# Kernel tuning notes

Hardware: AMD Instinct MI355X
Metric: run time of the kernel (lower is better)

## Reference

```python
import jax, jax.numpy as jnp
import numpy as np

N_NODES = 50000
N_EDGES = 800000
IN_F, H_F, OUT_F = 256, 256, 128


def setup_inputs() -> dict:
    key = jax.random.key(0)
    k1, k2, k3, k4, k5, k6 = jax.random.split(key, 6)
    in_feat = jax.random.normal(k1, (N_NODES, IN_F), dtype=jnp.float32)
    src = jax.random.randint(k2, (N_EDGES,), 0, N_NODES, dtype=jnp.int32)
    dst = jax.random.randint(k3, (N_EDGES,), 0, N_NODES, dtype=jnp.int32)
    s1 = 1.0 / np.sqrt(IN_F)
    s2 = 1.0 / np.sqrt(H_F)
    W1 = jax.random.uniform(k4, (IN_F, H_F), dtype=jnp.float32, minval=-s1, maxval=s1)
    b1 = jnp.zeros((H_F,), dtype=jnp.float32)
    W2 = jax.random.uniform(k5, (H_F, OUT_F), dtype=jnp.float32, minval=-s2, maxval=s2)
    b2 = jnp.zeros((OUT_F,), dtype=jnp.float32)
    return {"in_feat": in_feat, "src": src, "dst": dst,
            "W1": W1, "b1": b1, "W2": W2, "b2": b2}


def _graph_conv(x, W, b, src, dst, n_nodes):
    # DGL GraphConv with norm='both':
    #   h = D_in^{-1/2} A D_out^{-1/2} (X W) + b   (degrees clamped to min 1)
    ones = jnp.ones((src.shape[0],), dtype=x.dtype)
    deg_out = jax.ops.segment_sum(ones, src, num_segments=n_nodes)
    deg_in = jax.ops.segment_sum(ones, dst, num_segments=n_nodes)
    norm_out = jax.lax.rsqrt(jnp.maximum(deg_out, 1.0))  # [N]
    norm_in = jax.lax.rsqrt(jnp.maximum(deg_in, 1.0))    # [N]
    h = (x @ W) * norm_out[:, None]                       # [N, F_out]
    agg = jax.ops.segment_sum(h[src], dst, num_segments=n_nodes)  # SpMM
    return agg * norm_in[:, None] + b


def reference(in_feat, src, dst, W1, b1, W2, b2):
    n = in_feat.shape[0]
    h = _graph_conv(in_feat, W1, b1, src, dst, n)
    h = jax.nn.relu(h)
    h = _graph_conv(h, W2, b2, src, dst, n)
    # dgl.mean_nodes over a single graph -> mean across all nodes
    return jnp.mean(h, axis=0)  # [OUT_F]
```

## Files before the change

### kernel.cpp

```cpp
#include <hip/hip_runtime.h>


#define NNODES 50000
#define NEDGES 800000
#define CH      64
#define EPC     (NEDGES / CH)
#define NVEC    12
#define TAILB   (NVEC * 1024)
#define TAILN   (EPC - TAILB)
#define HWORDS  12500
#define QN      12500
#define G1_BM   ((NNODES + 127) / 128)
#define MEGA_NB 768
#define WS_NB   1536
#define NQUAD   (NNODES / 4)

typedef __bf16 bf16x8 __attribute__((ext_vector_type(8)));
typedef float f32x4 __attribute__((ext_vector_type(4)));
typedef float f32x2 __attribute__((ext_vector_type(2)));

__device__ __forceinline__ unsigned short f2b(float f) {
    union { float f; unsigned u; } v; v.f = f;
    unsigned r = 0x7fffu + ((v.u >> 16) & 1u);
    return (unsigned short)((v.u + r) >> 16);
}
__device__ __forceinline__ unsigned char f2fp8(float x) {
    return (unsigned char)(__builtin_amdgcn_cvt_pk_fp8_f32(x, x, 0, false) & 0xff);
}
__device__ __forceinline__ float rdeg(int d) {
    return __frsqrt_rn((float)max(d, 1));
}

__global__ __launch_bounds__(256) void k_hist0(
    const float* __restrict__ W1, unsigned short* __restrict__ W1t,
    const int* __restrict__ src, const int* __restrict__ dst,
    unsigned* __restrict__ degInP,
    unsigned* __restrict__ degOutP)
{
    __shared__ unsigned lds[HWORDS];
    int bid = blockIdx.x, tid = threadIdx.x;

    if (bid < 256) {
        int id = bid * 256 + tid;
        int k = id >> 8, n = id & 255;
        W1t[n * 256 + k] = f2b(W1[id]);
        return;
    }

    int b = bid - 256;
    const int* key = (b < 128) ? dst : src;
    unsigned* outP = (b < 128) ? degInP : degOutP;
    int b2 = b & 127;
    int c = b2 >> 1, h = b2 & 1;
    int lo = h * 25000;

    for (int i = tid; i < HWORDS; i += 256) lds[i] = 0;
    __syncthreads();
    int base = c * EPC;
    for (int i = 0; i < NVEC; i++) {
        int e = base + (i * 256 + tid) * 4;
        int4 k4 = *(const int4*)&key[e];
        int kk[4] = {k4.x, k4.y, k4.z, k4.w};
#pragma unroll
        for (int u = 0; u < 4; u++) {
            unsigned r = (unsigned)(kk[u] - lo);
            if (r < 25000u) atomicAdd(&lds[r >> 1], 1u << ((r & 1) * 16));
        }
    }
    if (tid < TAILN) {
        unsigned r = (unsigned)(key[base + TAILB + tid] - lo);
        if (r < 25000u) atomicAdd(&lds[r >> 1], 1u << ((r & 1) * 16));
    }
    __syncthreads();
    unsigned* op = outP + (size_t)b2 * HWORDS;
    for (int i = tid; i < HWORDS; i += 256) op[i] = lds[i];
}

__global__ __launch_bounds__(256) void k_merge0(
    const unsigned* __restrict__ degInP, const unsigned* __restrict__ degOutP,
    unsigned* __restrict__ chunkStartPk,
    float* __restrict__ normIn, float* __restrict__ normOut,
    int* __restrict__ degc)
{
    int id = blockIdx.x * blockDim.x + threadIdx.x;
    if (id >= 25000) return;
    int h = id >= HWORDS, w = id - h * HWORDS;
    unsigned runLo = 0, runHi = 0, oLo = 0, oHi = 0;
#pragma unroll 8
    for (int c = 0; c < CH; c++) {
        size_t idx = (size_t)(c * 2 + h) * HWORDS + w;
        unsigned x = degInP[idx];
        chunkStartPk[idx] = runLo | (runHi << 16);
        runLo += x & 0xffffu; runHi += x >> 16;
        unsigned y = degOutP[idx];
        oLo += y & 0xffffu; oHi += y >> 16;
    }
    int d0 = h * 25000 + 2 * w, d1 = d0 + 1;
    normIn[d0] = rdeg((int)runLo);  normIn[d1] = rdeg((int)runHi);
    normOut[d0] = rdeg((int)oLo);   normOut[d1] = rdeg((int)oHi);
    degc[d0] = min((int)runLo, 64); degc[d1] = min((int)runHi, 64);
}

__global__ __launch_bounds__(256) void k_mega2(
    const int* __restrict__ src, const int* __restrict__ dst,
    const unsigned* __restrict__ chunkStartPk,
    unsigned short* __restrict__ col2,
    const float* __restrict__ normIn, const float* __restrict__ normOut,
    float* __restrict__ wsumP,
    const float* __restrict__ X, const unsigned short* __restrict__ W1t,
    unsigned char* __restrict__ H, int M)
{
    __shared__ __align__(16) unsigned char smem[50048];
    int bid = blockIdx.x, tid = threadIdx.x;

    if (bid < 128) {
        unsigned* cntL = (unsigned*)smem;
        int c = bid >> 1, h = bid & 1;
        int lo = h * 25000;
        const unsigned* cs = chunkStartPk + (size_t)(c * 2 + h) * HWORDS;
        for (int i = tid; i < HWORDS; i += 256) cntL[i] = cs[i];
        __syncthreads();
        int base = c * EPC;
        for (int i = 0; i < NVEC; i++) {
            int e = base + (i * 256 + tid) * 4;
            int4 d4 = *(const int4*)&dst[e];
            int4 s4 = *(const int4*)&src[e];
            int dd[4] = {d4.x, d4.y, d4.z, d4.w};
            int ss[4] = {s4.x, s4.y, s4.z, s4.w};
#pragma unroll
            for (int u = 0; u < 4; u++) {
                unsigned r = (unsigned)(dd[u] - lo);
                if (r < 25000u) {
                    unsigned sh = (r & 1) * 16;
                    unsigned wv = atomicAdd(&cntL[r >> 1], 1u << sh);
                    unsigned slot = (wv >> sh) & 0xffffu;
                    if (slot < 64) col2[(size_t)dd[u] * 64 + slot] = (unsigned short)ss[u];
                }
            }
        }
        if (tid < TAILN) {
            int e = base + TAILB + tid;
            int d = dst[e];
            unsigned r = (unsigned)(d - lo);
            if (r < 25000u) {
                int s = src[e];
                unsigned sh = (r & 1) * 16;
                unsigned wv = atomicAdd(&cntL[r >> 1], 1u << sh);
                unsigned slot = (wv >> sh) & 0xffffu;
                if (slot < 64) col2[(size_t)d * 64 + slot] = (unsigned short)s;
            }
        }
        return;
    }

    if (bid < 384) {
        float* wf = (float*)smem;
        int b2 = bid - 128;
        int c = b2 >> 2, q = b2 & 3;
        int lo = q * QN;
        for (int i = tid; i < QN; i += 256) wf[i] = 0.f;
        __syncthreads();
        int base = c * EPC;
        for (int i = 0; i < NVEC; i++) {
            int e = base + (i * 256 + tid) * 4;
            int4 s4 = *(const int4*)&src[e];
            int4 d4 = *(const int4*)&dst[e];
            int ss[4] = {s4.x, s4.y, s4.z, s4.w};
            int dd[4] = {d4.x, d4.y, d4.z, d4.w};
#pragma unroll
            for (int u = 0; u < 4; u++) {
                unsigned r = (unsigned)(ss[u] - lo);
                if (r < (unsigned)QN) {
                    float ni = normIn[dd[u]];
                    atomicAdd(&wf[r], ni);
                }
            }
        }
        if (tid < TAILN) {
            int e = base + TAILB + tid;
            unsigned r = (unsigned)(src[e] - lo);
            if (r < (unsigned)QN) atomicAdd(&wf[r], normIn[dst[e]]);
        }
        __syncthreads();
        float* op = wsumP + (size_t)b2 * QN;
        for (int i = tid; i < QN; i += 256) op[i] = wf[i];
        return;
    }

    unsigned short (*As)[40] = (unsigned short (*)[40])smem;
    unsigned short (*Bs)[40] = (unsigned short (*)[40])(smem + 10240);
    int lane = tid & 63, wave = tid >> 6;
    int wm = (wave >> 1) * 64, wn = (wave & 1) * 64;
    int q = lane >> 4, r16 = lane & 15;
    int c0 = tid, c1 = tid + 256;
    int r0 = c0 >> 2, k0c = (c0 & 3) * 8;
    int r1 = c1 >> 2, k1c = (c1 & 3) * 8;

    auto pk2u = [](float a, float b) -> unsigned {
        unsigned short x = f2b(a), y = f2b(b);
        return (unsigned)x | ((unsigned)y << 16);
    };

    for (int g = bid - 384; g < 2 * G1_BM; g += MEGA_NB - 384) {
        int bm = g % G1_BM, bn = g / G1_BM;
        int m0 = bm * 128, n0 = bn * 128;

        f32x4 acc[4][4];
#pragma unroll
        for (int i = 0; i < 4; i++)
#pragma unroll
            for (int j = 0; j < 4; j++) acc[i][j] = 0.f;

        const float* Ar0 = X + (size_t)min(m0 + r0, M - 1) * 256;
        const float* Ar1 = X + (size_t)min(m0 + r1, M - 1) * 256;
        const unsigned short* Br0 = W1t + (size_t)(n0 + r0) * 256;
        const unsigned short* Br1 = W1t + (size_t)(n0 + r1) * 256;

        for (int k0 = 0; k0 < 256; k0 += 32) {
            float4 fa0 = *(const float4*)(Ar0 + k0 + k0c);
            float4 fa1 = *(const float4*)(Ar0 + k0 + k0c + 4);
            float4 fb0 = *(const float4*)(Ar1 + k0 + k1c);
            float4 fb1 = *(const float4*)(Ar1 + k0 + k1c + 4);
            uint4 vb0 = *(const uint4*)(Br0 + k0 + k0c);
            uint4 vb1 = *(const uint4*)(Br1 + k0 + k1c);
            uint4 va0 = make_uint4(pk2u(fa0.x, fa0.y), pk2u(fa0.z, fa0.w), pk2u(fa1.x, fa1.y), pk2u(fa1.z, fa1.w));
            uint4 va1 = make_uint4(pk2u(fb0.x, fb0.y), pk2u(fb0.z, fb0.w), pk2u(fb1.x, fb1.y), pk2u(fb1.z, fb1.w));
            __syncthreads();
            *(uint4*)&As[r0][k0c] = va0;
            *(uint4*)&As[r1][k1c] = va1;
            *(uint4*)&Bs[r0][k0c] = vb0;
            *(uint4*)&Bs[r1][k1c] = vb1;
            __syncthreads();
            bf16x8 af[4], bf[4];
#pragma unroll
            for (int i = 0; i < 4; i++)
                af[i] = *(const bf16x8*)&As[wm + i * 16 + r16][q * 8];
#pragma unroll
            for (int j = 0; j < 4; j++)
                bf[j] = *(const bf16x8*)&Bs[wn + j * 16 + r16][q * 8];
#pragma unroll
            for (int i = 0; i < 4; i++)
#pragma unroll
                for (int j = 0; j < 4; j++)
                    acc[i][j] = __builtin_amdgcn_mfma_f32_16x16x32_bf16(af[i], bf[j], acc[i][j], 0, 0, 0);
        }

#pragma unroll
        for (int i = 0; i < 4; i++) {
#pragma unroll
            for (int rr = 0; rr < 4; rr++) {
                int m = m0 + wm + i * 16 + q * 4 + rr;
                if (m < M) {
                    float no = normOut[m];
                    unsigned char* Hp = H + (size_t)m * 256 + n0 + wn + r16;
#pragma unroll
                    for (int j = 0; j < 4; j++)
                        Hp[j * 16] = f2fp8(acc[i][j][rr] * no);
                }
            }
        }
    }
}

__global__ __launch_bounds__(256) void k_merge1(
    const float* __restrict__ wsumP, const float* __restrict__ normOut,
    const float* __restrict__ normIn, const int* __restrict__ degc,
    float4* __restrict__ meta)
{
    int i = blockIdx.x * blockDim.x + threadIdx.x;
    if (i >= NNODES) return;
    int q = i / QN, li = i - q * QN;
    float ws = 0.f;
#pragma unroll 8
    for (int c = 0; c < CH; c++) ws += wsumP[(size_t)(c * 4 + q) * QN + li];
    meta[i] = make_float4(normOut[i] * ws, normIn[i],
                          __int_as_float(degc[i]), 0.f);
}

__global__ __launch_bounds__(256) void k_spmm_wsum(
    const unsigned char* __restrict__ H, const float4* __restrict__ meta,
    const unsigned short* __restrict__ col2,
    const float* __restrict__ bias, float* __restrict__ vpart) {
    __shared__ float sm[4][256];
    int wave = threadIdx.x >> 6;
    int lane = threadIdx.x & 63;
    int f = lane * 4;
    const unsigned char* Hf = H + f;
    float4 bv = *(const float4*)(bias + f);
    float vac0 = 0.f, vac1 = 0.f, vac2 = 0.f, vac3 = 0.f;

    int qd = blockIdx.x;
    int node = qd * 4 + wave;
    float4 pM = make_float4(0.f, 0.f, 0.f, 0.f);
    int pc = 0;
    if (qd < NQUAD) {
        pM = meta[node];
        pc = (int)col2[(size_t)node * 64 + lane];
    }

    while (qd < NQUAD) {
        float wn = pM.x, nI = pM.y;
        int dI = __float_as_int(pM.z), myc = pc;

        int nqd = qd + gridDim.x;
        if (nqd < NQUAD) {
            int nn = nqd * 4 + wave;
            pM = meta[nn];
            pc = (int)col2[(size_t)nn * 64 + lane];
        }

        float a0 = 0.f, a1 = 0.f, a2 = 0.f, a3 = 0.f;
        int i = 0;
        for (; i + 16 <= dI; i += 16) {
            unsigned v[16];
#pragma unroll
            for (int u = 0; u < 16; u++) {
                int c = __builtin_amdgcn_readlane(myc, i + u);
                v[u] = *(const unsigned*)(Hf + (size_t)c * 256);
            }
#pragma unroll
            for (int u = 0; u < 16; u++) {
                f32x2 lo = __builtin_amdgcn_cvt_pk_f32_fp8(v[u], false);
                f32x2 hi = __builtin_amdgcn_cvt_pk_f32_fp8(v[u], true);
                a0 += lo.x; a1 += lo.y; a2 += hi.x; a3 += hi.y;
            }
        }
        for (; i + 4 <= dI; i += 4) {
            unsigned v[4];
#pragma unroll
            for (int u = 0; u < 4; u++) {
                int c = __builtin_amdgcn_readlane(myc, i + u);
                v[u] = *(const unsigned*)(Hf + (size_t)c * 256);
            }
#pragma unroll
            for (int u = 0; u < 4; u++) {
                f32x2 lo = __builtin_amdgcn_cvt_pk_f32_fp8(v[u], false);
                f32x2 hi = __builtin_amdgcn_cvt_pk_f32_fp8(v[u], true);
                a0 += lo.x; a1 += lo.y; a2 += hi.x; a3 += hi.y;
            }
        }
        for (; i < dI; i++) {
            int c = __builtin_amdgcn_readlane(myc, i);
            unsigned v = *(const unsigned*)(Hf + (size_t)c * 256);
            f32x2 lo = __builtin_amdgcn_cvt_pk_f32_fp8(v, false);
            f32x2 hi = __builtin_amdgcn_cvt_pk_f32_fp8(v, true);
            a0 += lo.x; a1 += lo.y; a2 += hi.x; a3 += hi.y;
        }

        vac0 += wn * fmaxf(a0 * nI + bv.x, 0.f);
        vac1 += wn * fmaxf(a1 * nI + bv.y, 0.f);
        vac2 += wn * fmaxf(a2 * nI + bv.z, 0.f);
        vac3 += wn * fmaxf(a3 * nI + bv.w, 0.f);

        qd = nqd;
    }

    *(float4*)&sm[wave][f] = make_float4(vac0, vac1, vac2, vac3);
    __syncthreads();
    int t = threadIdx.x;
    float s4 = sm[0][t] + sm[1][t] + sm[2][t] + sm[3][t];
    vpart[(size_t)blockIdx.x * 256 + t] = s4;
}

__global__ __launch_bounds__(256) void k_red1(const float* __restrict__ vpart,
                                              float* __restrict__ vred) {
    int b = blockIdx.x;
    int t = threadIdx.x;
    float s = 0.f;
    for (int i = b; i < WS_NB; i += 64) s += vpart[(size_t)i * 256 + t];
    vred[(size_t)b * 256 + t] = s;
}

__global__ __launch_bounds__(1024) void k_final(
    const float* __restrict__ vred, const float* __restrict__ W2,
    const float* __restrict__ b2, float* __restrict__ out) {
    __shared__ float part[4][256];
    __shared__ float v[256];
    int t = threadIdx.x;
    int feat = t & 255, pr = t >> 8;
    float s = 0.f;
    for (int i = pr; i < 64; i += 4) s += vred[(size_t)i * 256 + feat];
    part[pr][feat] = s;
    __syncthreads();
    if (t < 256) v[t] = part[0][t] + part[1][t] + part[2][t] + part[3][t];
    __syncthreads();
    if (t < 128) {
        float o = 0.f;
        for (int k = 0; k < 256; k++) o += v[k] * W2[k * 128 + t];
        out[t] = o * (1.0f / (float)NNODES) + b2[t];
    }
}

extern "C" void kernel_launch(void* const* d_in, const int* in_sizes, int n_in,
                              void* d_out, int out_size, void* d_ws, size_t ws_size,
                              hipStream_t stream) {
    const float* X   = (const float*)d_in[0];
    const int*   src = (const int*)d_in[1];
    const int*   dst = (const int*)d_in[2];
    const float* W1  = (const float*)d_in[3];
    const float* b1  = (const float*)d_in[4];
    const float* W2  = (const float*)d_in[5];
    const float* b2  = (const float*)d_in[6];
    float* out = (float*)d_out;

    const int n = NNODES;

    char* p = (char*)d_ws;
    auto carve = [&](size_t bytes) -> void* {
        void* r = (void*)p;
        p += (bytes + 255) & ~(size_t)255;
        return r;
    };
    unsigned short* col2 = (unsigned short*)carve((size_t)n * 64 * 2);
    unsigned short* W1t  = (unsigned short*)carve((size_t)256 * 256 * 2);
    unsigned char*  bufA = (unsigned char*)carve((size_t)n * 256);
    float* normIn  = (float*)carve((size_t)n * sizeof(float));
    float* normOut = (float*)carve((size_t)n * sizeof(float));
    int*   degc    = (int*)carve((size_t)n * sizeof(int));
    float4* meta   = (float4*)carve((size_t)n * sizeof(float4));
    size_t histP_bytes = (size_t)128 * HWORDS * sizeof(unsigned);
    char* histr = (char*)carve(2 * histP_bytes);
    unsigned* degInP  = (unsigned*)histr;
    unsigned* degOutP = (unsigned*)(histr + histP_bytes);
    float*    wsumP   = (float*)histr;
    char* csr = (char*)carve(histP_bytes);
    unsigned* chunkStartPk = (unsigned*)csr;
    float* vpart = (float*)csr;
    float* vred  = (float*)(csr + (size_t)WS_NB * 256 * sizeof(float));

    k_hist0<<<512, 256, 0, stream>>>(W1, W1t, src, dst, degInP, degOutP);

    k_merge0<<<98, 256, 0, stream>>>(degInP, degOutP, chunkStartPk,
                                     normIn, normOut, degc);

    k_mega2<<<MEGA_NB, 256, 0, stream>>>(
        src, dst, chunkStartPk, col2, normIn, normOut, wsumP, X, W1t, bufA, n);

    k_merge1<<<(n + 255) / 256, 256, 0, stream>>>(wsumP, normOut, normIn, degc, meta);

    k_spmm_wsum<<<WS_NB, 256, 0, stream>>>(bufA, meta, col2, b1, vpart);

    k_red1<<<64, 256, 0, stream>>>(vpart, vred);
    k_final<<<1, 1024, 0, stream>>>(vred, W2, b2, out);
}
```

Baseline: 214.3 us.

## Partition SpMM gather into source-range passes and give GEMM one tile per block

The SpMM kernel now gives each block up to 8 node-quads and makes 4 passes over their neighbour lists. Each pass gathers only source rows from one quarter of the node range, so the working set of H per pass is smaller and more likely to stay in cache. The GEMM part of the mega kernel drops its grid-stride loop and launches enough blocks for one output tile each. The cost is redundant readlane and predicate work across passes and more registers for the 8 accumulators, which can lower occupancy. Per-iteration loads are also predicated and no longer batched, which reduces memory-level parallelism.

```diff
diff --git a/kernel.cpp b/kernel.cpp
--- a/kernel.cpp
+++ b/kernel.cpp
@@ -11,9 +11,11 @@
 #define HWORDS  12500
 #define QN      12500
 #define G1_BM   ((NNODES + 127) / 128)
-#define MEGA_NB 768
-#define WS_NB   1536
+#define MEGA_NB (128 + 256 + 2 * G1_BM)
+#define WS_NB   1563
 #define NQUAD   (NNODES / 4)
+#define NPASS   4
+#define PQ      12500
 
 typedef __bf16 bf16x8 __attribute__((ext_vector_type(8)));
 typedef float f32x4 __attribute__((ext_vector_type(4)));
@@ -189,74 +191,72 @@
 
     unsigned short (*As)[40] = (unsigned short (*)[40])smem;
     unsigned short (*Bs)[40] = (unsigned short (*)[40])(smem + 10240);
+    int g = bid - 384;
+    int bm = g % G1_BM, bn = g / G1_BM;
+    int m0 = bm * 128, n0 = bn * 128;
     int lane = tid & 63, wave = tid >> 6;
     int wm = (wave >> 1) * 64, wn = (wave & 1) * 64;
     int q = lane >> 4, r16 = lane & 15;
+
+    f32x4 acc[4][4];
+#pragma unroll
+    for (int i = 0; i < 4; i++)
+#pragma unroll
+        for (int j = 0; j < 4; j++) acc[i][j] = 0.f;
+
     int c0 = tid, c1 = tid + 256;
     int r0 = c0 >> 2, k0c = (c0 & 3) * 8;
     int r1 = c1 >> 2, k1c = (c1 & 3) * 8;
+    const float* Ar0 = X + (size_t)min(m0 + r0, M - 1) * 256;
+    const float* Ar1 = X + (size_t)min(m0 + r1, M - 1) * 256;
+    const unsigned short* Br0 = W1t + (size_t)(n0 + r0) * 256;
+    const unsigned short* Br1 = W1t + (size_t)(n0 + r1) * 256;
 
     auto pk2u = [](float a, float b) -> unsigned {
         unsigned short x = f2b(a), y = f2b(b);
         return (unsigned)x | ((unsigned)y << 16);
     };
 
-    for (int g = bid - 384; g < 2 * G1_BM; g += MEGA_NB - 384) {
-        int bm = g % G1_BM, bn = g / G1_BM;
-        int m0 = bm * 128, n0 = bn * 128;
-
-        f32x4 acc[4][4];
+    for (int k0 = 0; k0 < 256; k0 += 32) {
+        float4 fa0 = *(const float4*)(Ar0 + k0 + k0c);
+        float4 fa1 = *(const float4*)(Ar0 + k0 + k0c + 4);
+        float4 fb0 = *(const float4*)(Ar1 + k0 + k1c);
+        float4 fb1 = *(const float4*)(Ar1 + k0 + k1c + 4);
+        uint4 vb0 = *(const uint4*)(Br0 + k0 + k0c);
+        uint4 vb1 = *(const uint4*)(Br1 + k0 + k1c);
+        uint4 va0 = make_uint4(pk2u(fa0.x, fa0.y), pk2u(fa0.z, fa0.w), pk2u(fa1.x, fa1.y), pk2u(fa1.z, fa1.w));
+        uint4 va1 = make_uint4(pk2u(fb0.x, fb0.y), pk2u(fb0.z, fb0.w), pk2u(fb1.x, fb1.y), pk2u(fb1.z, fb1.w));
+        __syncthreads();
+        *(uint4*)&As[r0][k0c] = va0;
+        *(uint4*)&As[r1][k1c] = va1;
+        *(uint4*)&Bs[r0][k0c] = vb0;
+        *(uint4*)&Bs[r1][k1c] = vb1;
+        __syncthreads();
+        bf16x8 af[4], bf[4];
 #pragma unroll
         for (int i = 0; i < 4; i++)
-#pragma unroll
-            for (int j = 0; j < 4; j++) acc[i][j] = 0.f;
-
-        const float* Ar0 = X + (size_t)min(m0 + r0, M - 1) * 256;
-        const float* Ar1 = X + (size_t)min(m0 + r1, M - 1) * 256;
-        const unsigned short* Br0 = W1t + (size_t)(n0 + r0) * 256;
-        const unsigned short* Br1 = W1t + (size_t)(n0 + r1) * 256;
-
-        for (int k0 = 0; k0 < 256; k0 += 32) {
-            float4 fa0 = *(const float4*)(Ar0 + k0 + k0c);
-            float4 fa1 = *(const float4*)(Ar0 + k0 + k0c + 4);
-            float4 fb0 = *(const float4*)(Ar1 + k0 + k1c);
-            float4 fb1 = *(const float4*)(Ar1 + k0 + k1c + 4);
-            uint4 vb0 = *(const uint4*)(Br0 + k0 + k0c);
-            uint4 vb1 = *(const uint4*)(Br1 + k0 + k1c);
-            uint4 va0 = make_uint4(pk2u(fa0.x, fa0.y), pk2u(fa0.z, fa0.w), pk2u(fa1.x, fa1.y), pk2u(fa1.z, fa1.w));
-            uint4 va1 = make_uint4(pk2u(fb0.x, fb0.y), pk2u(fb0.z, fb0.w), pk2u(fb1.x, fb1.y), pk2u(fb1.z, fb1.w));
-            __syncthreads();
-            *(uint4*)&As[r0][k0c] = va0;
-            *(uint4*)&As[r1][k1c] = va1;
-            *(uint4*)&Bs[r0][k0c] = vb0;
-            *(uint4*)&Bs[r1][k1c] = vb1;
-            __syncthreads();
-            bf16x8 af[4], bf[4];
-#pragma unroll
-            for (int i = 0; i < 4; i++)
-                af[i] = *(const bf16x8*)&As[wm + i * 16 + r16][q * 8];
+            af[i] = *(const bf16x8*)&As[wm + i * 16 + r16][q * 8];
+#pragma unroll
+        for (int j = 0; j < 4; j++)
+            bf[j] = *(const bf16x8*)&Bs[wn + j * 16 + r16][q * 8];
+#pragma unroll
+        for (int i = 0; i < 4; i++)
 #pragma unroll
             for (int j = 0; j < 4; j++)
-                bf[j] = *(const bf16x8*)&Bs[wn + j * 16 + r16][q * 8];
-#pragma unroll
-            for (int i = 0; i < 4; i++)
+                acc[i][j] = __builtin_amdgcn_mfma_f32_16x16x32_bf16(af[i], bf[j], acc[i][j], 0, 0, 0);
+    }
+
+#pragma unroll
+    for (int i = 0; i < 4; i++) {
+#pragma unroll
+        for (int rr = 0; rr < 4; rr++) {
+            int m = m0 + wm + i * 16 + q * 4 + rr;
+            if (m < M) {
+                float no = normOut[m];
+                unsigned char* Hp = H + (size_t)m * 256 + n0 + wn + r16;
 #pragma unroll
                 for (int j = 0; j < 4; j++)
-                    acc[i][j] = __builtin_amdgcn_mfma_f32_16x16x32_bf16(af[i], bf[j], acc[i][j], 0, 0, 0);
-        }
-
-#pragma unroll
-        for (int i = 0; i < 4; i++) {
-#pragma unroll
-            for (int rr = 0; rr < 4; rr++) {
-                int m = m0 + wm + i * 16 + q * 4 + rr;
-                if (m < M) {
-                    float no = normOut[m];
-                    unsigned char* Hp = H + (size_t)m * 256 + n0 + wn + r16;
-#pragma unroll
-                    for (int j = 0; j < 4; j++)
-                        Hp[j * 16] = f2fp8(acc[i][j][rr] * no);
-                }
+                    Hp[j * 16] = f2fp8(acc[i][j][rr] * no);
             }
         }
     }
@@ -279,87 +279,75 @@
 
 __global__ __launch_bounds__(256) void k_spmm_wsum(
     const unsigned char* __restrict__ H, const float4* __restrict__ meta,
-    const unsigned short* __restrict__ col2,
+    const int* __restrict__ degc, const unsigned short* __restrict__ col2,
     const float* __restrict__ bias, float* __restrict__ vpart) {
     __shared__ float sm[4][256];
     int wave = threadIdx.x >> 6;
     int lane = threadIdx.x & 63;
     int f = lane * 4;
     const unsigned char* Hf = H + f;
+    int bid = blockIdx.x;
+
+    int colr[8];
+    int di[8];
+    float a[8][4];
+#pragma unroll
+    for (int qi = 0; qi < 8; qi++) {
+        int qd = bid + qi * WS_NB;
+        colr[qi] = 0; di[qi] = 0;
+        a[qi][0] = a[qi][1] = a[qi][2] = a[qi][3] = 0.f;
+        if (qd < NQUAD) {
+            int node = qd * 4 + wave;
+            di[qi] = degc[node];
+            colr[qi] = (int)col2[(size_t)node * 64 + lane];
+        }
+    }
+
+    for (int p = 0; p < NPASS; p++) {
+        int plo = p * PQ;
+#pragma unroll
+        for (int qi = 0; qi < 8; qi++) {
+            int dI = di[qi];
+            int myc = colr[qi];
+            for (int i = 0; i < dI; i += 16) {
+#pragma unroll
+                for (int u = 0; u < 16; u++) {
+                    if (i + u < dI) {
+                        int c = __builtin_amdgcn_readlane(myc, i + u);
+                        if ((unsigned)(c - plo) < (unsigned)PQ) {
+                            unsigned v = *(const unsigned*)(Hf + (size_t)c * 256);
+                            f32x2 l2 = __builtin_amdgcn_cvt_pk_f32_fp8(v, false);
+                            f32x2 h2 = __builtin_amdgcn_cvt_pk_f32_fp8(v, true);
+                            a[qi][0] += l2.x; a[qi][1] += l2.y;
+                            a[qi][2] += h2.x; a[qi][3] += h2.y;
+                        }
+                    }
+                }
+            }
+        }
+    }
+
     float4 bv = *(const float4*)(bias + f);
     float vac0 = 0.f, vac1 = 0.f, vac2 = 0.f, vac3 = 0.f;
-
-    int qd = blockIdx.x;
-    int node = qd * 4 + wave;
-    float4 pM = make_float4(0.f, 0.f, 0.f, 0.f);
-    int pc = 0;
-    if (qd < NQUAD) {
-        pM = meta[node];
-        pc = (int)col2[(size_t)node * 64 + lane];
-    }
-
-    while (qd < NQUAD) {
-        float wn = pM.x, nI = pM.y;
-        int dI = __float_as_int(pM.z), myc = pc;
-
-        int nqd = qd + gridDim.x;
-        if (nqd < NQUAD) {
-            int nn = nqd * 4 + wave;
-            pM = meta[nn];
-            pc = (int)col2[(size_t)nn * 64 + lane];
-        }
-
-        float a0 = 0.f, a1 = 0.f, a2 = 0.f, a3 = 0.f;
-        int i = 0;
-        for (; i + 16 <= dI; i += 16) {
-            unsigned v[16];
-#pragma unroll
-            for (int u = 0; u < 16; u++) {
-                int c = __builtin_amdgcn_readlane(myc, i + u);
-                v[u] = *(const unsigned*)(Hf + (size_t)c * 256);
-            }
-#pragma unroll
-            for (int u = 0; u < 16; u++) {
-                f32x2 lo = __builtin_amdgcn_cvt_pk_f32_fp8(v[u], false);
-                f32x2 hi = __builtin_amdgcn_cvt_pk_f32_fp8(v[u], true);
-                a0 += lo.x; a1 += lo.y; a2 += hi.x; a3 += hi.y;
-            }
-        }
-        for (; i + 4 <= dI; i += 4) {
-            unsigned v[4];
-#pragma unroll
-            for (int u = 0; u < 4; u++) {
-                int c = __builtin_amdgcn_readlane(myc, i + u);
-                v[u] = *(const unsigned*)(Hf + (size_t)c * 256);
-            }
-#pragma unroll
-            for (int u = 0; u < 4; u++) {
-                f32x2 lo = __builtin_amdgcn_cvt_pk_f32_fp8(v[u], false);
-                f32x2 hi = __builtin_amdgcn_cvt_pk_f32_fp8(v[u], true);
-                a0 += lo.x; a1 += lo.y; a2 += hi.x; a3 += hi.y;
-            }
-        }
-        for (; i < dI; i++) {
-            int c = __builtin_amdgcn_readlane(myc, i);
-            unsigned v = *(const unsigned*)(Hf + (size_t)c * 256);
-            f32x2 lo = __builtin_amdgcn_cvt_pk_f32_fp8(v, false);
-            f32x2 hi = __builtin_amdgcn_cvt_pk_f32_fp8(v, true);
-            a0 += lo.x; a1 += lo.y; a2 += hi.x; a3 += hi.y;
-        }
-
-        vac0 += wn * fmaxf(a0 * nI + bv.x, 0.f);
-        vac1 += wn * fmaxf(a1 * nI + bv.y, 0.f);
-        vac2 += wn * fmaxf(a2 * nI + bv.z, 0.f);
-        vac3 += wn * fmaxf(a3 * nI + bv.w, 0.f);
-
-        qd = nqd;
+#pragma unroll
+    for (int qi = 0; qi < 8; qi++) {
+        int qd = bid + qi * WS_NB;
+        if (qd < NQUAD) {
+            int node = qd * 4 + wave;
+            float4 pM = meta[node];
+            float wn = pM.x, nI = pM.y;
+            vac0 += wn * fmaxf(a[qi][0] * nI + bv.x, 0.f);
+            vac1 += wn * fmaxf(a[qi][1] * nI + bv.y, 0.f);
+            vac2 += wn * fmaxf(a[qi][2] * nI + bv.z, 0.f);
+            vac3 += wn * fmaxf(a[qi][3] * nI + bv.w, 0.f);
+        }
     }
 
     *(float4*)&sm[wave][f] = make_float4(vac0, vac1, vac2, vac3);
     __syncthreads();
     int t = threadIdx.x;
     float s4 = sm[0][t] + sm[1][t] + sm[2][t] + sm[3][t];
-    vpart[(size_t)blockIdx.x * 256 + t] = s4;
+    vpart[(size_t)bid * 256 + t] = s4;
 }
 
 __global__ __launch_bounds__(256) void k_red1(const float* __restrict__ vpart,
@@ -438,7 +426,7 @@
 
     k_merge1<<<(n + 255) / 256, 256, 0, stream>>>(wsumP, normOut, normIn, degc, meta);
 
-    k_spmm_wsum<<<WS_NB, 256, 0, stream>>>(bufA, meta, col2, b1, vpart);
+    k_spmm_wsum<<<WS_NB, 256, 0, stream>>>(bufA, meta, degc, col2, b1, vpart);
 
     k_red1<<<64, 256, 0, stream>>>(vpart, vred);
     k_final<<<1, 1024, 0, stream>>>(vred, W2, b2, out);
```

New measurement: 262.0 us. 1.22x slower.
